# Performance work log

Hardware: AMD Instinct MI355X
Metric: run time of the kernel (lower is better)

Reference implementation:

```python
import jax, jax.numpy as jnp
import numpy as np

ATTACK_RATE = 0.03

def setup_inputs() -> dict:
    key = jax.random.key(0)
    rec_audio = jax.random.normal(key, (256, 131072), dtype=jnp.float32)
    return {"rec_audio": rec_audio}

def reference(rec_audio):
    B, N = rec_audio.shape
    k = int(ATTACK_RATE * N)  # number of samples zeroed per row (without replacement)
    # Gumbel-trick style: per-row uniform scores; top-k scores pick k distinct indices,
    # equivalent to np.random.choice(replace=False) per row, fully vectorized.
    u = jax.random.uniform(jax.random.key(42), (B, N), dtype=jnp.float32)
    _, idx = jax.lax.top_k(u, k)                  # [B, k] distinct indices per row
    rows = jnp.arange(B)[:, None]                 # [B, 1]
    mask = jnp.ones((B, N), dtype=rec_audio.dtype).at[rows, idx].set(0.0)
    return rec_audio * mask
```

## Files before the change

kernel.cpp:

```cpp
#include <hip/hip_runtime.h>
#include <stdint.h>

#define NROWS 256
#define NCOLS 131072
#define KSEL  3932
#define TPB   1024
#define VITERS (NCOLS / (TPB * 4))
#define BINS  256
#define MAXC  1024

__device__ __forceinline__ uint32_t rotl32(uint32_t v, int r) {
    return __builtin_amdgcn_alignbit(v, v, 32 - r);
}

__device__ __forceinline__ uint32_t jax_bits(uint32_t j) {
    const uint32_t ks0 = 0u;
    const uint32_t ks1 = 42u;
    const uint32_t ks2 = ks0 ^ ks1 ^ 0x1BD11BDAu;
    uint32_t x0 = 0u + ks0;
    uint32_t x1 = j + ks1;
#define TF_RND(r) { x0 += x1; x1 = rotl32(x1, r); x1 ^= x0; }
    TF_RND(13) TF_RND(15) TF_RND(26) TF_RND(6)
    x0 += ks1; x1 += ks2 + 1u;
    TF_RND(17) TF_RND(29) TF_RND(16) TF_RND(24)
    x0 += ks2; x1 += ks0 + 2u;
    TF_RND(13) TF_RND(15) TF_RND(26) TF_RND(6)
    x0 += ks0; x1 += ks1 + 3u;
    TF_RND(17) TF_RND(29) TF_RND(16) TF_RND(24)
    x0 += ks1; x1 += ks2 + 4u;
    TF_RND(13) TF_RND(15) TF_RND(26) TF_RND(6)
    x0 += ks2; x1 += ks0 + 5u;
#undef TF_RND
    return x0 ^ x1;
}

__global__ __launch_bounds__(TPB) void topk_mask_kernel(const float* __restrict__ in,
                                                        float* __restrict__ out) {
    __shared__ uint32_t hist[BINS];
    __shared__ uint32_t scanb[BINS];
    __shared__ uint32_t ckeys[MAXC];
    __shared__ uint32_t s_ccount;
    __shared__ uint32_t s_bstar;
    __shared__ uint32_t s_r;
    __shared__ uint32_t s_tkey;

    const uint32_t row  = blockIdx.x;
    const uint32_t tid  = threadIdx.x;
    const uint32_t base = row * (uint32_t)NCOLS;

    uint32_t pk[VITERS];

    if (tid < BINS) hist[tid] = 0u;
    if (tid == 0) s_ccount = 0u;
    __syncthreads();

    #pragma unroll
    for (int it = 0; it < VITERS; ++it) {
        uint32_t vi = (uint32_t)it * TPB + tid;
        uint32_t j  = base + vi * 4u;
        uint32_t b0 = jax_bits(j + 0u);
        uint32_t b1 = jax_bits(j + 1u);
        uint32_t b2 = jax_bits(j + 2u);
        uint32_t b3 = jax_bits(j + 3u);
        atomicAdd(&hist[b0 >> 24], 1u);
        atomicAdd(&hist[b1 >> 24], 1u);
        atomicAdd(&hist[b2 >> 24], 1u);
        atomicAdd(&hist[b3 >> 24], 1u);
        pk[it] = (b0 >> 24) | ((b1 >> 24) << 8) | ((b2 >> 24) << 16) | ((b3 >> 24) << 24);
    }
    __syncthreads();

    uint32_t h = 0, S = 0;
    if (tid < BINS) { h = hist[tid]; scanb[tid] = h; }
    __syncthreads();
    S = h;
    for (uint32_t off = 1; off < BINS; off <<= 1) {
        uint32_t v = 0;
        if (tid < BINS && tid + off < BINS) v = scanb[tid + off];
        __syncthreads();
        if (tid < BINS) { S += v; scanb[tid] = S; }
        __syncthreads();
    }
    if (tid < BINS) {
        uint32_t above = S - h;
        if (above < KSEL && S >= KSEL) {
            s_bstar = tid;
            s_r = KSEL - above;
        }
    }
    __syncthreads();

    const uint32_t bstar = s_bstar;
    const uint32_t r     = s_r;

    const float4* in4  = (const float4*)(in + base);
    float4*       out4 = (float4*)(out + base);
    #pragma unroll
    for (int it = 0; it < VITERS; ++it) {
        uint32_t vi = (uint32_t)it * TPB + tid;
        uint32_t c  = vi * 4u;
        float4 v = in4[vi];
        uint32_t p = pk[it];
        float* pv = (float*)&v;
        #pragma unroll
        for (int e = 0; e < 4; ++e) {
            uint32_t bin = (p >> (8 * e)) & 0xFFu;
            if (bin > bstar) {
                pv[e] = 0.0f;
            } else if (bin == bstar) {
                uint32_t pos = atomicAdd(&s_ccount, 1u);
                if (pos < MAXC) ckeys[pos] = c + (uint32_t)e;
            }
        }
        out4[vi] = v;
    }
    __syncthreads();

    uint32_t cc = s_ccount; if (cc > MAXC) cc = MAXC;
    uint32_t mykey = 0, myc = 0;
    if (tid < cc) {
        myc = ckeys[tid];
        uint32_t bits = jax_bits(base + myc);
        mykey = (((bits >> 9) & 0x7FFFu) << 17) | (131071u - myc);
    }
    __syncthreads();
    if (tid < cc) ckeys[tid] = mykey;
    __syncthreads();

    if (tid < cc) {
        uint32_t rank = 0;
        for (uint32_t i = 0; i < cc; ++i) rank += (ckeys[i] > mykey) ? 1u : 0u;
        if (rank == r - 1) s_tkey = mykey;
    }
    __syncthreads();

    if (tid < cc && mykey >= s_tkey) {
        out[base + myc] = 0.0f;
    }
}

extern "C" void kernel_launch(void* const* d_in, const int* in_sizes, int n_in,
                              void* d_out, int out_size, void* d_ws, size_t ws_size,
                              hipStream_t stream) {
    const float* in = (const float*)d_in[0];
    float* out = (float*)d_out;
    hipLaunchKernelGGL(topk_mask_kernel, dim3(NROWS), dim3(TPB), 0, stream, in, out);
}
```

Baseline: 309.1 us.

## Prefilter candidates with fixed threshold and fuse copy into RNG pass

Replaces the two-pass approach (histogram over all 131072 values, then a masked copy) with a single pass. That pass copies the input to the output and, using a fixed mantissa threshold, collects a small candidate set of high random values into shared memory. A fine histogram, rank selection and scatter-zeroing then run only over those candidates. This removes the register-packed bins and the second streaming pass, and overlaps the memory copy with Threefry compute. It relies on the threshold always admitting at least k candidates and no more than MAXC per row. That assumption comes from the statistics of the fixed-seed random stream, and the code does not check it.

```diff
diff --git a/kernel.cpp b/kernel.cpp
--- a/kernel.cpp
+++ b/kernel.cpp
@@ -6,8 +6,10 @@
 #define KSEL  3932
 #define TPB   1024
 #define VITERS (NCOLS / (TPB * 4))
-#define BINS  256
-#define MAXC  1024
+#define TM    8106908u
+#define MAXC  5120
+#define SBINS 256
+#define MAXB  256
 
 __device__ __forceinline__ uint32_t rotl32(uint32_t v, int r) {
     return __builtin_amdgcn_alignbit(v, v, 32 - r);
@@ -36,10 +38,13 @@
 
 __global__ __launch_bounds__(TPB) void topk_mask_kernel(const float* __restrict__ in,
                                                         float* __restrict__ out) {
-    __shared__ uint32_t hist[BINS];
-    __shared__ uint32_t scanb[BINS];
-    __shared__ uint32_t ckeys[MAXC];
+    __shared__ uint32_t cm[MAXC];
+    __shared__ uint32_t cidx[MAXC];
+    __shared__ uint32_t hist[SBINS];
+    __shared__ uint32_t scanb[SBINS];
+    __shared__ uint32_t bkeys[MAXB];
     __shared__ uint32_t s_ccount;
+    __shared__ uint32_t s_bcnt;
     __shared__ uint32_t s_bstar;
     __shared__ uint32_t s_r;
     __shared__ uint32_t s_tkey;
@@ -48,40 +53,46 @@
     const uint32_t tid  = threadIdx.x;
     const uint32_t base = row * (uint32_t)NCOLS;
 
-    uint32_t pk[VITERS];
-
-    if (tid < BINS) hist[tid] = 0u;
-    if (tid == 0) s_ccount = 0u;
+    if (tid < SBINS) hist[tid] = 0u;
+    if (tid == 0) { s_ccount = 0u; s_bcnt = 0u; }
     __syncthreads();
 
-    #pragma unroll
+    const float4* in4  = (const float4*)(in + base);
+    float4*       out4 = (float4*)(out + base);
     for (int it = 0; it < VITERS; ++it) {
         uint32_t vi = (uint32_t)it * TPB + tid;
-        uint32_t j  = base + vi * 4u;
-        uint32_t b0 = jax_bits(j + 0u);
-        uint32_t b1 = jax_bits(j + 1u);
-        uint32_t b2 = jax_bits(j + 2u);
-        uint32_t b3 = jax_bits(j + 3u);
-        atomicAdd(&hist[b0 >> 24], 1u);
-        atomicAdd(&hist[b1 >> 24], 1u);
-        atomicAdd(&hist[b2 >> 24], 1u);
-        atomicAdd(&hist[b3 >> 24], 1u);
-        pk[it] = (b0 >> 24) | ((b1 >> 24) << 8) | ((b2 >> 24) << 16) | ((b3 >> 24) << 24);
+        uint32_t c  = vi * 4u;
+        uint32_t j  = base + c;
+        float4 v = in4[vi];
+        uint32_t m0 = jax_bits(j + 0u) >> 9;
+        uint32_t m1 = jax_bits(j + 1u) >> 9;
+        uint32_t m2 = jax_bits(j + 2u) >> 9;
+        uint32_t m3 = jax_bits(j + 3u) >> 9;
+        out4[vi] = v;
+        if (m0 >= TM) { uint32_t p = atomicAdd(&s_ccount, 1u); if (p < MAXC) { cm[p] = m0 - TM; cidx[p] = c + 0u; } }
+        if (m1 >= TM) { uint32_t p = atomicAdd(&s_ccount, 1u); if (p < MAXC) { cm[p] = m1 - TM; cidx[p] = c + 1u; } }
+        if (m2 >= TM) { uint32_t p = atomicAdd(&s_ccount, 1u); if (p < MAXC) { cm[p] = m2 - TM; cidx[p] = c + 2u; } }
+        if (m3 >= TM) { uint32_t p = atomicAdd(&s_ccount, 1u); if (p < MAXC) { cm[p] = m3 - TM; cidx[p] = c + 3u; } }
     }
     __syncthreads();
 
+    uint32_t cc = s_ccount; if (cc > MAXC) cc = MAXC;
+
+    for (uint32_t i = tid; i < cc; i += TPB) atomicAdd(&hist[cm[i] >> 11], 1u);
+    __syncthreads();
+
     uint32_t h = 0, S = 0;
-    if (tid < BINS) { h = hist[tid]; scanb[tid] = h; }
+    if (tid < SBINS) { h = hist[tid]; scanb[tid] = h; }
     __syncthreads();
     S = h;
-    for (uint32_t off = 1; off < BINS; off <<= 1) {
+    for (uint32_t off = 1; off < SBINS; off <<= 1) {
         uint32_t v = 0;
-        if (tid < BINS && tid + off < BINS) v = scanb[tid + off];
+        if (tid < SBINS && tid + off < SBINS) v = scanb[tid + off];
         __syncthreads();
-        if (tid < BINS) { S += v; scanb[tid] = S; }
+        if (tid < SBINS) { S += v; scanb[tid] = S; }
         __syncthreads();
     }
-    if (tid < BINS) {
+    if (tid < SBINS) {
         uint32_t above = S - h;
         if (above < KSEL && S >= KSEL) {
             s_bstar = tid;
@@ -93,49 +104,33 @@
     const uint32_t bstar = s_bstar;
     const uint32_t r     = s_r;
 
-    const float4* in4  = (const float4*)(in + base);
-    float4*       out4 = (float4*)(out + base);
-    #pragma unroll
-    for (int it = 0; it < VITERS; ++it) {
-        uint32_t vi = (uint32_t)it * TPB + tid;
-        uint32_t c  = vi * 4u;
-        float4 v = in4[vi];
-        uint32_t p = pk[it];
-        float* pv = (float*)&v;
-        #pragma unroll
-        for (int e = 0; e < 4; ++e) {
-            uint32_t bin = (p >> (8 * e)) & 0xFFu;
-            if (bin > bstar) {
-                pv[e] = 0.0f;
-            } else if (bin == bstar) {
-                uint32_t pos = atomicAdd(&s_ccount, 1u);
-                if (pos < MAXC) ckeys[pos] = c + (uint32_t)e;
-            }
+    for (uint32_t i = tid; i < cc; i += TPB) {
+        if ((cm[i] >> 11) == bstar) {
+            uint32_t p = atomicAdd(&s_bcnt, 1u);
+            if (p < MAXB) bkeys[p] = ((cm[i] & 2047u) << 17) | (131071u - cidx[i]);
         }
-        out4[vi] = v;
     }
     __syncthreads();
 
-    uint32_t cc = s_ccount; if (cc > MAXC) cc = MAXC;
-    uint32_t mykey = 0, myc = 0;
-    if (tid < cc) {
-        myc = ckeys[tid];
-        uint32_t bits = jax_bits(base + myc);
-        mykey = (((bits >> 9) & 0x7FFFu) << 17) | (131071u - myc);
-    }
-    __syncthreads();
-    if (tid < cc) ckeys[tid] = mykey;
-    __syncthreads();
-
-    if (tid < cc) {
+    uint32_t bc = s_bcnt; if (bc > MAXB) bc = MAXB;
+    if (tid < bc) {
+        uint32_t mykey = bkeys[tid];
         uint32_t rank = 0;
-        for (uint32_t i = 0; i < cc; ++i) rank += (ckeys[i] > mykey) ? 1u : 0u;
+        for (uint32_t i = 0; i < bc; ++i) rank += (bkeys[i] > mykey) ? 1u : 0u;
         if (rank == r - 1) s_tkey = mykey;
     }
     __syncthreads();
 
-    if (tid < cc && mykey >= s_tkey) {
-        out[base + myc] = 0.0f;
+    const uint32_t tkey = s_tkey;
+
+    for (uint32_t i = tid; i < cc; i += TPB) {
+        uint32_t bin = cm[i] >> 11;
+        bool z = (bin > bstar);
+        if (bin == bstar) {
+            uint32_t key = ((cm[i] & 2047u) << 17) | (131071u - cidx[i]);
+            z = (key >= tkey);
+        }
+        if (z) out[base + cidx[i]] = 0.0f;
     }
 }
 
```

Result: faster. 295.9 us (-4.3%).
